# Performance work log

Hardware: AMD Instinct MI355X
Metric: run time of the kernel (lower is better)

Reference implementation:

```python
import jax, jax.numpy as jnp
import numpy as np

N, E, B = 3000, 96000, 64
CIN, MID = 8, 16
G1, G2 = 32, 8
FC1, FC2, OUT = 512, 128, 10
EPS = 1e-5


def setup_inputs() -> dict:
    key = jax.random.key(0)
    ks = jax.random.split(key, 40)
    u = lambda k, shape, s: jax.random.uniform(k, shape, jnp.float32, -s, s)
    inp = {}
    inp['x'] = jax.random.normal(ks[0], (N, B, CIN), jnp.float32)
    inp['edge_index'] = jax.random.randint(ks[1], (2, E), 0, N, jnp.int64)
    # SAGEConv params (uniform(-1/sqrt(in_channels), ...))
    s = 1.0 / np.sqrt(CIN)
    inp['edge_w_raw'] = jnp.ones((E,), jnp.float32) * 0.01
    inp['sage_self_w'] = u(ks[2], (CIN, MID), s)
    inp['sage_w'] = u(ks[3], (CIN, MID), s)
    inp['sage_b'] = u(ks[4], (MID,), s)
    # LayerNorm over (num_nodes, mid_channel)
    inp['ln_g'] = jnp.ones((N, MID), jnp.float32)
    inp['ln_b'] = jnp.zeros((N, MID), jnp.float32)
    # 1x1 Conv2d stacks (stored as [out,in] matrices) + BatchNorm2d (eval stats)
    inp['conv1_w'] = jax.random.normal(ks[5], (G1, MID), jnp.float32) * np.sqrt(2.0 / G1)
    inp['conv1_b'] = u(ks[6], (G1,), 1.0 / np.sqrt(MID))
    inp['bn1_g'] = jax.random.uniform(ks[7], (G1,), jnp.float32, 0.5, 1.5)
    inp['bn1_b'] = jax.random.normal(ks[8], (G1,), jnp.float32) * 0.1
    inp['bn1_m'] = jax.random.normal(ks[9], (G1,), jnp.float32) * 0.1
    inp['bn1_v'] = jax.random.uniform(ks[10], (G1,), jnp.float32, 0.5, 1.5)
    inp['conv2_w'] = jax.random.normal(ks[11], (G2, G1), jnp.float32) * np.sqrt(2.0 / G2)
    inp['conv2_b'] = u(ks[12], (G2,), 1.0 / np.sqrt(G1))
    inp['bn2_g'] = jax.random.uniform(ks[13], (G2,), jnp.float32, 0.5, 1.5)
    inp['bn2_b'] = jax.random.normal(ks[14], (G2,), jnp.float32) * 0.1
    inp['bn2_m'] = jax.random.normal(ks[15], (G2,), jnp.float32) * 0.1
    inp['bn2_v'] = jax.random.uniform(ks[16], (G2,), jnp.float32, 0.5, 1.5)
    # FC stack: Linear(G2*N, FC1) + BN1d, Linear(FC1, FC2) + BN1d, fc1
    d0 = G2 * N
    inp['fc_w1'] = jax.random.normal(ks[17], (FC1, d0), jnp.float32) * np.sqrt(2.0 / (d0 + FC1))
    inp['fc_b1'] = jnp.full((FC1,), 0.01, jnp.float32)
    inp['bnf1_g'] = jax.random.uniform(ks[18], (FC1,), jnp.float32, 0.5, 1.5)
    inp['bnf1_b'] = jax.random.normal(ks[19], (FC1,), jnp.float32) * 0.1
    inp['bnf1_m'] = jax.random.normal(ks[20], (FC1,), jnp.float32) * 0.1
    inp['bnf1_v'] = jax.random.uniform(ks[21], (FC1,), jnp.float32, 0.5, 1.5)
    inp['fc_w2'] = jax.random.normal(ks[22], (FC2, FC1), jnp.float32) * np.sqrt(2.0 / (FC1 + FC2))
    inp['fc_b2'] = jnp.full((FC2,), 0.01, jnp.float32)
    inp['bnf2_g'] = jax.random.uniform(ks[23], (FC2,), jnp.float32, 0.5, 1.5)
    inp['bnf2_b'] = jax.random.normal(ks[24], (FC2,), jnp.float32) * 0.1
    inp['bnf2_m'] = jax.random.normal(ks[25], (FC2,), jnp.float32) * 0.1
    inp['bnf2_v'] = jax.random.uniform(ks[26], (FC2,), jnp.float32, 0.5, 1.5)
    inp['fc1_w'] = jax.random.normal(ks[27], (OUT, FC2), jnp.float32) * np.sqrt(2.0 / (FC2 + OUT))
    inp['fc1_b'] = jnp.full((OUT,), 0.01, jnp.float32)
    return inp


def _bn(y, g, b, m, v):
    # eval-mode BatchNorm; y is [B, C, N] or [B, C]
    if y.ndim == 3:
        return (y - m[:, None]) * (g[:, None] / jnp.sqrt(v[:, None] + EPS)) + b[:, None]
    return (y - m) * (g / jnp.sqrt(v + EPS)) + b


def reference(x, edge_index, edge_w_raw, sage_self_w, sage_w, sage_b, ln_g, ln_b,
              conv1_w, conv1_b, bn1_g, bn1_b, bn1_m, bn1_v,
              conv2_w, conv2_b, bn2_g, bn2_b, bn2_m, bn2_v,
              fc_w1, fc_b1, bnf1_g, bnf1_b, bnf1_m, bnf1_v,
              fc_w2, fc_b2, bnf2_g, bnf2_b, bnf2_m, bnf2_v,
              fc1_w, fc1_b):
    row, col = edge_index[0], edge_index[1]
    ew = jax.nn.sigmoid(edge_w_raw)
    # SAGEConv: gather -> weighted message -> scatter-mean by col -> matmul
    msg = x[row] * ew[:, None, None]                          # [E, B, CIN]
    summed = jax.ops.segment_sum(msg, col, num_segments=N)    # [N, B, CIN]
    cnt = jax.ops.segment_sum(jnp.ones((E,), x.dtype), col, num_segments=N)
    agg = summed / jnp.maximum(cnt, 1.0)[:, None, None]
    neigh = jnp.einsum('nbc,cm->nbm', agg, sage_w) + sage_b   # [N, B, MID]
    self_out = jnp.einsum('nbc,cm->nbm', x, sage_self_w)
    h = 0.0 * self_out + 1.0 * neigh                          # alphas = [0, 1]
    h = jax.nn.relu(h)
    # LayerNorm over (num_nodes, mid) per batch element
    hb = jnp.transpose(h, (1, 0, 2))                          # [B, N, MID]
    mu = hb.mean(axis=(1, 2), keepdims=True)
    var = hb.var(axis=(1, 2), keepdims=True)
    hb = (hb - mu) / jnp.sqrt(var + EPS) * ln_g + ln_b
    y = jnp.transpose(hb, (0, 2, 1))                          # [B, MID, N]
    # 1x1 conv stack (relu then BN, matching source order)
    y = jnp.einsum('om,bmn->bon', conv1_w, y) + conv1_b[:, None]
    y = _bn(jax.nn.relu(y), bn1_g, bn1_b, bn1_m, bn1_v)
    y = jnp.einsum('oc,bcn->bon', conv2_w, y) + conv2_b[:, None]
    y = _bn(jax.nn.relu(y), bn2_g, bn2_b, bn2_m, bn2_v)       # [B, G2, N]
    z = y.reshape(y.shape[0], -1)                             # [B, G2*N]
    z = jax.nn.relu(_bn(z @ fc_w1.T + fc_b1, bnf1_g, bnf1_b, bnf1_m, bnf1_v))
    z = jax.nn.relu(_bn(z @ fc_w2.T + fc_b2, bnf2_g, bnf2_b, bnf2_m, bnf2_v))
    logits = z @ fc1_w.T + fc1_b
    return jax.nn.softmax(logits, axis=-1), logits
```

## Files before the change

kernel.cpp:

```cpp
#include <hip/hip_runtime.h>
#include <hip/hip_bf16.h>
#include <math.h>

#define NN   3000
#define EE   96000
#define BB   64
#define CIN  8
#define MID  16
#define G1   32
#define G2   8
#define FC1N 512
#define FC2N 128
#define OUTN 10
#define EPSV 1e-5f

#define BC   (BB * CIN)
#define HROW (NN * MID)
#define D0   (G2 * NN)

#define P_EWRAW 0
#define P_SW    96000
#define P_SB    96128
#define P_LNG   96144
#define P_LNB   144144
#define P_C1W   192144
#define P_C1B   192656
#define P_BN1G  192688
#define P_BN1B  192720
#define P_BN1M  192752
#define P_BN1V  192784
#define P_C2W   192816
#define P_C2B   193072
#define P_BN2G  193080
#define P_BN2B  193088
#define P_BN2M  193096
#define P_BN2V  193104
#define P_FB1   193112
#define P_BF1G  193624
#define P_BF1B  194136
#define P_BF1M  194648
#define P_BF1V  195160
#define P_FW2   195672
#define P_FB2   261208
#define P_BF2G  261336
#define P_BF2B  261464
#define P_BF2M  261592
#define P_BF2V  261720
#define P_FOW   261848
#define P_FOB   263128
#define P_TOT   263138

#define KCH  320
#define NKC  75
#define SK   32

__device__ __forceinline__ float b2f(unsigned short u) {
    union { unsigned int i; float f; } c;
    c.i = ((unsigned int)u) << 16;
    return c.f;
}

typedef __attribute__((ext_vector_type(8))) unsigned short us8;

__global__ void k_prep(const void* __restrict__ ei_raw,
                       const unsigned int* __restrict__ ewr,
                       int* __restrict__ ei32, int* __restrict__ cnt,
                       int* __restrict__ flags) {
    __shared__ int is64;
    if (threadIdx.x == 0) {
        const int* p = (const int*)ei_raw;
        int any = 0;
        #pragma unroll
        for (int i = 1; i < 32; i += 2) any |= p[i];
        is64 = (any == 0) ? 1 : 0;
        if (blockIdx.x == 0) {
            unsigned int w = ewr[0];
            flags[0] = ((w >> 16) == (w & 0xFFFFu)) ? 1 : 0;
        }
    }
    __syncthreads();
    int i = blockIdx.x * blockDim.x + threadIdx.x;
    if (i < 2 * EE) {
        int v = is64 ? (int)((const long long*)ei_raw)[i]
                     : ((const int*)ei_raw)[i];
        ei32[i] = v;
        if (i >= EE) atomicAdd(&cnt[v], 1);
    }
}

struct PTab { const void* p[30]; };
__global__ __launch_bounds__(256)
void k_cvt_all(PTab tab, const void* __restrict__ xr,
               const int* __restrict__ flags,
               float* __restrict__ x32, float* __restrict__ P) {
    int i = blockIdx.x * blockDim.x + threadIdx.x;
    int bf = flags[0];
    if (i < NN * BC) {
        x32[i] = bf ? b2f(((const unsigned short*)xr)[i]) : ((const float*)xr)[i];
        return;
    }
    i -= NN * BC;
    if (i >= P_TOT) return;
    const int off[31] = {
        P_EWRAW, P_SW, P_SB, P_LNG, P_LNB, P_C1W, P_C1B, P_BN1G, P_BN1B, P_BN1M,
        P_BN1V, P_C2W, P_C2B, P_BN2G, P_BN2B, P_BN2M, P_BN2V, P_FB1, P_BF1G,
        P_BF1B, P_BF1M, P_BF1V, P_FW2, P_FB2, P_BF2G, P_BF2B, P_BF2M, P_BF2V,
        P_FOW, P_FOB, P_TOT };
    int r = 0;
    #pragma unroll
    for (int j = 1; j < 31; ++j) r += (i >= off[j]) ? 1 : 0;
    int e = i - off[r];
    P[i] = bf ? b2f(((const unsigned short*)tab.p[r])[e])
              : ((const float*)tab.p[r])[e];
}

__global__ void k_scan(const int* __restrict__ cnt, int* __restrict__ off,
                       int* __restrict__ cursor) {
    __shared__ int part[1024];
    int t = threadIdx.x;
    int base = t * 3;
    int c0 = 0, c1 = 0, c2 = 0;
    if (base     < NN) c0 = cnt[base];
    if (base + 1 < NN) c1 = cnt[base + 1];
    if (base + 2 < NN) c2 = cnt[base + 2];
    int s = c0 + c1 + c2;
    part[t] = s;
    __syncthreads();
    for (int d = 1; d < 1024; d <<= 1) {
        int v = (t >= d) ? part[t - d] : 0;
        __syncthreads();
        part[t] += v;
        __syncthreads();
    }
    int excl = part[t] - s;
    if (base < NN)     { off[base]     = excl;           cursor[base]     = excl; }
    if (base + 1 < NN) { off[base + 1] = excl + c0;      cursor[base + 1] = excl + c0; }
    if (base + 2 < NN) { off[base + 2] = excl + c0 + c1; cursor[base + 2] = excl + c0 + c1; }
    if (t == 1023) off[NN] = part[1023];
}

__global__ void k_scatter(const int* __restrict__ ei, const float* __restrict__ ew,
                          int* __restrict__ cursor,
                          int* __restrict__ rcsr, float* __restrict__ wcsr) {
    int e = blockIdx.x * blockDim.x + threadIdx.x;
    if (e < EE) {
        int p = atomicAdd(&cursor[ei[EE + e]], 1);
        rcsr[p] = ei[e];
        wcsr[p] = 1.f / (1.f + expf(-ew[e]));
    }
}

__global__ __launch_bounds__(256)
void k_agg_sage(const float* __restrict__ x,
                const int* __restrict__ off,
                const int* __restrict__ rcsr, const float* __restrict__ wcsr,
                const float* __restrict__ sw, const float* __restrict__ sb,
                float* __restrict__ hb) {
    __shared__ float aggL[BC];
    __shared__ float swL[CIN * MID];
    __shared__ float sbL[MID];
    int n = blockIdx.x;
    int t = threadIdx.x;
    if (t < CIN * MID) swL[t] = sw[t];
    if (t < MID)       sbL[t] = sb[t];
    int k0 = off[n], k1 = off[n + 1];
    float a0 = 0.f, a1 = 0.f, b0 = 0.f, b1 = 0.f;
    int k = k0;
    for (; k + 1 < k1; k += 2) {
        int   r0 = rcsr[k],   r1 = rcsr[k + 1];
        float w0 = wcsr[k],   w1 = wcsr[k + 1];
        const float* xp0 = x + (size_t)r0 * BC;
        const float* xp1 = x + (size_t)r1 * BC;
        a0 += xp0[t]       * w0;
        a1 += xp0[t + 256] * w0;
        b0 += xp1[t]       * w1;
        b1 += xp1[t + 256] * w1;
    }
    if (k < k1) {
        int r0 = rcsr[k];
        float w0 = wcsr[k];
        const float* xp0 = x + (size_t)r0 * BC;
        a0 += xp0[t] * w0;
        a1 += xp0[t + 256] * w0;
    }
    float inv = 1.f / fmaxf((float)(k1 - k0), 1.f);
    aggL[t]       = (a0 + b0) * inv;
    aggL[t + 256] = (a1 + b1) * inv;
    __syncthreads();
    #pragma unroll
    for (int r4 = 0; r4 < 4; ++r4) {
        int q = t + r4 * 256;
        int b = q >> 4, m = q & 15;
        float v = sbL[m];
        const float* ag = &aggL[b * CIN];
        #pragma unroll
        for (int c = 0; c < CIN; ++c) v += ag[c] * swL[c * MID + m];
        v = fmaxf(v, 0.f);
        hb[(size_t)b * HROW + n * MID + m] = v;
    }
}

__global__ __launch_bounds__(256)
void k_ln_stats(const float* __restrict__ hb, float* __restrict__ stats) {
    __shared__ float ssum[256], ssq[256];
    int b = blockIdx.x, t = threadIdx.x;
    const float4* p = (const float4*)(hb + (size_t)b * HROW);
    float s = 0.f, q = 0.f;
    for (int i = t; i < HROW / 4; i += 256) {
        float4 v = p[i];
        s += v.x + v.y + v.z + v.w;
        q += v.x * v.x + v.y * v.y + v.z * v.z + v.w * v.w;
    }
    ssum[t] = s; ssq[t] = q;
    __syncthreads();
    for (int d = 128; d > 0; d >>= 1) {
        if (t < d) { ssum[t] += ssum[t + d]; ssq[t] += ssq[t + d]; }
        __syncthreads();
    }
    if (t == 0) {
        float mu = ssum[0] / (float)HROW;
        float var = ssq[0] / (float)HROW - mu * mu;
        stats[b]      = mu;
        stats[BB + b] = 1.f / sqrtf(var + EPSV);
    }
}

__global__ __launch_bounds__(256)
void k_conv_stack(const float* __restrict__ hb, const float* __restrict__ stats,
                  const float* __restrict__ P, float* __restrict__ zT) {
    __shared__ float hbt[64 * 65];
    __shared__ float w1s[G1 * MID], w2s[G2 * G1];
    __shared__ float c1s[G1], s1[G1], t1[G1];
    __shared__ float c2s[G2], s2[G2], t2[G2];
    int t = threadIdx.x;
    int n0 = blockIdx.x * 4;
    for (int j = t; j < G1 * MID; j += 256) w1s[j] = P[P_C1W + j];
    if (t < G2 * G1)  w2s[t] = P[P_C2W + t];
    if (t < G1) {
        float s = P[P_BN1G + t] / sqrtf(P[P_BN1V + t] + EPSV);
        c1s[t] = P[P_C1B + t]; s1[t] = s; t1[t] = P[P_BN1B + t] - P[P_BN1M + t] * s;
    }
    if (t < G2) {
        float s = P[P_BN2G + t] / sqrtf(P[P_BN2V + t] + EPSV);
        c2s[t] = P[P_C2B + t]; s2[t] = s; t2[t] = P[P_BN2B + t] - P[P_BN2M + t] * s;
    }
    #pragma unroll
    for (int r = 0; r < 4; ++r) {
        int i = r * 256 + t;
        int b = i >> 4, q = i & 15;
        float4 v = *(const float4*)(hb + (size_t)b * HROW + n0 * MID + q * 4);
        int ld = b * 65 + q * 4;
        hbt[ld] = v.x; hbt[ld + 1] = v.y; hbt[ld + 2] = v.z; hbt[ld + 3] = v.w;
    }
    __syncthreads();
    int nl = t >> 6, b = t & 63;
    int n = n0 + nl;
    float mu = stats[b], rs = stats[BB + b];
    float tv[MID];
    #pragma unroll
    for (int m = 0; m < MID; ++m) {
        float g = P[P_LNG + n * MID + m], lb = P[P_LNB + n * MID + m];
        tv[m] = (hbt[b * 65 + nl * MID + m] - mu) * rs * g + lb;
    }
    float v1[G1];
    #pragma unroll
    for (int o = 0; o < G1; ++o) {
        float d = c1s[o];
        #pragma unroll
        for (int m = 0; m < MID; ++m) d += w1s[o * MID + m] * tv[m];
        d = fmaxf(d, 0.f);
        v1[o] = d * s1[o] + t1[o];
    }
    #pragma unroll
    for (int o2 = 0; o2 < G2; ++o2) {
        float d = c2s[o2];
        #pragma unroll
        for (int c = 0; c < G1; ++c) d += w2s[o2 * G1 + c] * v1[c];
        d = fmaxf(d, 0.f);
        zT[((size_t)(o2 * NN + n)) * BB + b] = d * s2[o2] + t2[o2];
    }
}

__global__ __launch_bounds__(256)
void k_fc1(const float* __restrict__ zT, const void* __restrict__ w1raw,
           const int* __restrict__ flags, float* __restrict__ out1p) {
    __shared__ float ws[32 * 40];
    __shared__ float zs[SK * 64];
    int fg = blockIdx.x, kc = blockIdx.y;
    int t = threadIdx.x;
    int fs2 = t >> 4, bq = t & 15;
    int f0 = fg * 32;
    int bf = flags[0];
    const float*          w1f = (const float*)w1raw;
    const unsigned short* w1b = (const unsigned short*)w1raw;
    const size_t kcb = (size_t)kc * KCH;

    float a[8];
    #pragma unroll
    for (int i = 0; i < 8; ++i) a[i] = 0.f;

    for (int step = 0; step < KCH / SK; ++step) {
        int kbase = step * SK;
        if (bf) {
            if (t < 128) {
                int row = t >> 2, kq8 = t & 3;
                us8 wv = *(const us8*)(w1b + (size_t)(f0 + row) * D0 + kcb + kbase + kq8 * 8);
                #pragma unroll
                for (int c = 0; c < 8; ++c) ws[row * 40 + kq8 * 8 + c] = b2f(wv[c]);
            }
        } else {
            int row = t >> 3, kq = t & 7;
            *(float4*)&ws[row * 40 + kq * 4] =
                *(const float4*)(w1f + (size_t)(f0 + row) * D0 + kcb + kbase + kq * 4);
        }
        const float* zsrc = zT + (kcb + kbase) * BB;
        *(float4*)&zs[t * 8]     = *(const float4*)(zsrc + t * 8);
        *(float4*)&zs[t * 8 + 4] = *(const float4*)(zsrc + t * 8 + 4);
        __syncthreads();
        #pragma unroll
        for (int k4 = 0; k4 < SK / 4; ++k4) {
            float4 w0 = *(const float4*)&ws[(fs2 * 2    ) * 40 + k4 * 4];
            float4 w1 = *(const float4*)&ws[(fs2 * 2 + 1) * 40 + k4 * 4];
            float4 z0 = *(const float4*)&zs[(k4 * 4    ) * 64 + bq * 4];
            float4 z1 = *(const float4*)&zs[(k4 * 4 + 1) * 64 + bq * 4];
            float4 z2 = *(const float4*)&zs[(k4 * 4 + 2) * 64 + bq * 4];
            float4 z3 = *(const float4*)&zs[(k4 * 4 + 3) * 64 + bq * 4];
            a[0] += w0.x * z0.x + w0.y * z1.x + w0.z * z2.x + w0.w * z3.x;
            a[1] += w0.x * z0.y + w0.y * z1.y + w0.z * z2.y + w0.w * z3.y;
            a[2] += w0.x * z0.z + w0.y * z1.z + w0.z * z2.z + w0.w * z3.z;
            a[3] += w0.x * z0.w + w0.y * z1.w + w0.z * z2.w + w0.w * z3.w;
            a[4] += w1.x * z0.x + w1.y * z1.x + w1.z * z2.x + w1.w * z3.x;
            a[5] += w1.x * z0.y + w1.y * z1.y + w1.z * z2.y + w1.w * z3.y;
            a[6] += w1.x * z0.z + w1.y * z1.z + w1.z * z2.z + w1.w * z3.z;
            a[7] += w1.x * z0.w + w1.y * z1.w + w1.z * z2.w + w1.w * z3.w;
        }
        __syncthreads();
    }
    float* op = out1p + ((size_t)kc * FC1N + f0 + fs2 * 2) * BB + bq * 4;
    *(float4*)op        = make_float4(a[0], a[1], a[2], a[3]);
    *(float4*)(op + BB) = make_float4(a[4], a[5], a[6], a[7]);
}

__global__ void k_fc1_fin(const float* __restrict__ out1p, const float* __restrict__ P,
                          float* __restrict__ z1) {
    int i = blockIdx.x * blockDim.x + threadIdx.x;
    if (i < BB * FC1N) {
        int f = i >> 6, b = i & 63;
        float acc = 0.f;
        for (int kc = 0; kc < NKC; ++kc)
            acc += out1p[((size_t)kc * FC1N + f) * BB + b];
        acc += P[P_FB1 + f];
        float s = P[P_BF1G + f] / sqrtf(P[P_BF1V + f] + EPSV);
        acc = (acc - P[P_BF1M + f]) * s + P[P_BF1B + f];
        z1[b * FC1N + f] = fmaxf(acc, 0.f);
    }
}

__global__ __launch_bounds__(128)
void k_fc2head(const float* __restrict__ z1, const float* __restrict__ P,
               const int* __restrict__ flags, void* __restrict__ outv) {
    __shared__ float zsrc[FC1N];
    __shared__ float z2s[FC2N];
    __shared__ float lg[OUTN];
    __shared__ float red[2];
    int b = blockIdx.x, t = threadIdx.x;
    #pragma unroll
    for (int r = 0; r < 4; ++r) zsrc[t + r * 128] = z1[b * FC1N + t + r * 128];
    __syncthreads();
    {
        int f = t;
        const float4* wr = (const float4*)(P + P_FW2 + (size_t)f * FC1N);
        const float4* zr = (const float4*)zsrc;
        float acc = P[P_FB2 + f];
        for (int k = 0; k < FC1N / 4; ++k) {
            float4 wv = wr[k];
            float4 zv = zr[k];
            acc += wv.x * zv.x + wv.y * zv.y + wv.z * zv.z + wv.w * zv.w;
        }
        float s = P[P_BF2G + f] / sqrtf(P[P_BF2V + f] + EPSV);
        acc = (acc - P[P_BF2M + f]) * s + P[P_BF2B + f];
        z2s[f] = fmaxf(acc, 0.f);
    }
    __syncthreads();
    if (t < OUTN) {
        float acc = P[P_FOB + t];
        const float* wr = P + P_FOW + t * FC2N;
        for (int k = 0; k < FC2N; ++k) acc += wr[k] * z2s[k];
        lg[t] = acc;
    }
    __syncthreads();
    if (t == 0) {
        float mx = lg[0];
        for (int o = 1; o < OUTN; ++o) mx = fmaxf(mx, lg[o]);
        float s = 0.f;
        for (int o = 0; o < OUTN; ++o) s += expf(lg[o] - mx);
        red[0] = mx; red[1] = s;
    }
    __syncthreads();
    if (t < OUTN) {
        float p = expf(lg[t] - red[0]) / red[1];
        if (flags[0]) {
            __hip_bfloat16* o = (__hip_bfloat16*)outv;
            o[b * OUTN + t] = __float2bfloat16(p);
            o[BB * OUTN + b * OUTN + t] = __float2bfloat16(lg[t]);
        } else {
            float* o = (float*)outv;
            o[b * OUTN + t] = p;
            o[BB * OUTN + b * OUTN + t] = lg[t];
        }
    }
}

extern "C" void kernel_launch(void* const* d_in, const int* in_sizes, int n_in,
                              void* d_out, int out_size, void* d_ws, size_t ws_size,
                              hipStream_t stream) {
    char* ws = (char*)d_ws;
    size_t o = 0;
    auto carve = [&](size_t bytes) { void* p = ws + o; o += (bytes + 255) & ~(size_t)255; return p; };
    int*   flags  = (int*)  carve(16);
    int*   ei32   = (int*)  carve((size_t)2 * EE * sizeof(int));
    int*   cnt    = (int*)  carve(NN * sizeof(int));
    int*   off    = (int*)  carve((NN + 1) * sizeof(int));
    int*   cursor = (int*)  carve(NN * sizeof(int));
    int*   rcsr   = (int*)  carve(EE * sizeof(int));
    float* wcsr   = (float*)carve(EE * sizeof(float));
    float* P      = (float*)carve((size_t)P_TOT * sizeof(float));
    float* x32    = (float*)carve((size_t)NN * BC * sizeof(float));
    float* hb     = (float*)carve((size_t)BB * HROW * sizeof(float));
    float* stats  = (float*)carve(2 * BB * sizeof(float));
    float* zT     = (float*)carve((size_t)D0 * BB * sizeof(float));
    float* out1p  = (float*)carve((size_t)NKC * FC1N * BB * sizeof(float));
    float* z1     = (float*)carve(BB * FC1N * sizeof(float));

    hipMemsetAsync(cnt, 0, NN * sizeof(int), stream);

    k_prep<<<(2 * EE + 255) / 256, 256, 0, stream>>>(d_in[1], (const unsigned int*)d_in[2],
                                                     ei32, cnt, flags);

    PTab tab;
    tab.p[0]  = d_in[2];   tab.p[1]  = d_in[4];   tab.p[2]  = d_in[5];
    tab.p[3]  = d_in[6];   tab.p[4]  = d_in[7];   tab.p[5]  = d_in[8];
    tab.p[6]  = d_in[9];   tab.p[7]  = d_in[10];  tab.p[8]  = d_in[11];
    tab.p[9]  = d_in[12];  tab.p[10] = d_in[13];  tab.p[11] = d_in[14];
    tab.p[12] = d_in[15];  tab.p[13] = d_in[16];  tab.p[14] = d_in[17];
    tab.p[15] = d_in[18];  tab.p[16] = d_in[19];  tab.p[17] = d_in[21];
    tab.p[18] = d_in[22];  tab.p[19] = d_in[23];  tab.p[20] = d_in[24];
    tab.p[21] = d_in[25];  tab.p[22] = d_in[26];  tab.p[23] = d_in[27];
    tab.p[24] = d_in[28];  tab.p[25] = d_in[29];  tab.p[26] = d_in[30];
    tab.p[27] = d_in[31];  tab.p[28] = d_in[32];  tab.p[29] = d_in[33];
    int cvt_tot = NN * BC + P_TOT;
    k_cvt_all<<<(cvt_tot + 255) / 256, 256, 0, stream>>>(tab, d_in[0], flags, x32, P);

    k_scan   <<<1, 1024, 0, stream>>>(cnt, off, cursor);
    k_scatter<<<(EE + 255) / 256, 256, 0, stream>>>(ei32, P + P_EWRAW, cursor, rcsr, wcsr);
    k_agg_sage<<<NN, 256, 0, stream>>>(x32, off, rcsr, wcsr, P + P_SW, P + P_SB, hb);
    k_ln_stats<<<BB, 256, 0, stream>>>(hb, stats);
    k_conv_stack<<<NN / 4, 256, 0, stream>>>(hb, stats, P, zT);
    dim3 g7(FC1N / 32, NKC);
    k_fc1    <<<g7, 256, 0, stream>>>(zT, d_in[20], flags, out1p);
    k_fc1_fin<<<(BB * FC1N + 255) / 256, 256, 0, stream>>>(out1p, P, z1);
    k_fc2head<<<BB, 128, 0, stream>>>(z1, P, flags, (void*)d_out);
}
```

Baseline: 281.0 us.

## Rewrite FC1 as register-tiled wave GEMM, fuse prep kernels, unroll aggregation

FC1 no longer uses a shared-memory tiled loop. Each wave now holds 64 z values per lane in registers and accumulates 32 output features, reading weight rows through uniform per-wave loads, with a new K-chunk split (192 wide, 125 chunks). The edge-index prep and the input/parameter conversion kernels are merged into one launch, which removes a launch and the flags read. The neighbour aggregation loop is unrolled by four to put more independent gathers in flight. The register-heavy FC1 (64 z values plus 32 accumulators) may lower occupancy, and the larger partial-sum buffer adds work to the reduction in k_fc1_fin.

```diff
diff --git a/kernel.cpp b/kernel.cpp
--- a/kernel.cpp
+++ b/kernel.cpp
@@ -50,9 +50,8 @@
 #define P_FOB   263128
 #define P_TOT   263138
 
-#define KCH  320
-#define NKC  75
-#define SK   32
+#define KCH  192
+#define NKC  125
 
 __device__ __forceinline__ float b2f(unsigned short u) {
     union { unsigned int i; float f; } c;
@@ -60,47 +59,43 @@
     return c.f;
 }
 
-typedef __attribute__((ext_vector_type(8))) unsigned short us8;
-
-__global__ void k_prep(const void* __restrict__ ei_raw,
-                       const unsigned int* __restrict__ ewr,
-                       int* __restrict__ ei32, int* __restrict__ cnt,
-                       int* __restrict__ flags) {
-    __shared__ int is64;
+struct PTab { const void* p[30]; };
+__global__ __launch_bounds__(256)
+void k_prep(const void* __restrict__ ei_raw, const unsigned int* __restrict__ ewr,
+            const void* __restrict__ xr, PTab tab,
+            int* __restrict__ ei32, int* __restrict__ cnt, int* __restrict__ flags,
+            float* __restrict__ x32, float* __restrict__ P) {
+    __shared__ int sh_is64, sh_bf;
     if (threadIdx.x == 0) {
-        const int* p = (const int*)ei_raw;
+        const int* pw = (const int*)ei_raw;
         int any = 0;
         #pragma unroll
-        for (int i = 1; i < 32; i += 2) any |= p[i];
-        is64 = (any == 0) ? 1 : 0;
-        if (blockIdx.x == 0) {
-            unsigned int w = ewr[0];
-            flags[0] = ((w >> 16) == (w & 0xFFFFu)) ? 1 : 0;
-        }
-    }
-    __syncthreads();
-    int i = blockIdx.x * blockDim.x + threadIdx.x;
-    if (i < 2 * EE) {
-        int v = is64 ? (int)((const long long*)ei_raw)[i]
-                     : ((const int*)ei_raw)[i];
+        for (int i = 1; i < 32; i += 2) any |= pw[i];
+        sh_is64 = (any == 0) ? 1 : 0;
+        unsigned int w = ewr[0];
+        sh_bf = ((w >> 16) == (w & 0xFFFFu)) ? 1 : 0;
+        if (blockIdx.x == 0) flags[0] = sh_bf;
+    }
+    __syncthreads();
+    int bf = sh_bf;
+    long long gi = (long long)blockIdx.x * blockDim.x + threadIdx.x;
+    if (gi < 2 * EE) {
+        int i = (int)gi;
+        int v = sh_is64 ? (int)((const long long*)ei_raw)[i]
+                        : ((const int*)ei_raw)[i];
         ei32[i] = v;
         if (i >= EE) atomicAdd(&cnt[v], 1);
-    }
-}
-
-struct PTab { const void* p[30]; };
-__global__ __launch_bounds__(256)
-void k_cvt_all(PTab tab, const void* __restrict__ xr,
-               const int* __restrict__ flags,
-               float* __restrict__ x32, float* __restrict__ P) {
-    int i = blockIdx.x * blockDim.x + threadIdx.x;
-    int bf = flags[0];
-    if (i < NN * BC) {
+        return;
+    }
+    gi -= 2 * EE;
+    if (gi < NN * BC) {
+        int i = (int)gi;
         x32[i] = bf ? b2f(((const unsigned short*)xr)[i]) : ((const float*)xr)[i];
         return;
     }
-    i -= NN * BC;
-    if (i >= P_TOT) return;
+    gi -= NN * BC;
+    if (gi >= P_TOT) return;
+    int i = (int)gi;
     const int off[31] = {
         P_EWRAW, P_SW, P_SB, P_LNG, P_LNB, P_C1W, P_C1B, P_BN1G, P_BN1B, P_BN1M,
         P_BN1V, P_C2W, P_C2B, P_BN2G, P_BN2B, P_BN2M, P_BN2V, P_FB1, P_BF1G,
@@ -166,17 +161,21 @@
     int k0 = off[n], k1 = off[n + 1];
     float a0 = 0.f, a1 = 0.f, b0 = 0.f, b1 = 0.f;
     int k = k0;
-    for (; k + 1 < k1; k += 2) {
-        int   r0 = rcsr[k],   r1 = rcsr[k + 1];
-        float w0 = wcsr[k],   w1 = wcsr[k + 1];
+    for (; k + 3 < k1; k += 4) {
+        int   r0 = rcsr[k],     r1 = rcsr[k + 1];
+        int   r2 = rcsr[k + 2], r3 = rcsr[k + 3];
+        float w0 = wcsr[k],     w1 = wcsr[k + 1];
+        float w2 = wcsr[k + 2], w3 = wcsr[k + 3];
         const float* xp0 = x + (size_t)r0 * BC;
         const float* xp1 = x + (size_t)r1 * BC;
-        a0 += xp0[t]       * w0;
-        a1 += xp0[t + 256] * w0;
-        b0 += xp1[t]       * w1;
-        b1 += xp1[t + 256] * w1;
-    }
-    if (k < k1) {
+        const float* xp2 = x + (size_t)r2 * BC;
+        const float* xp3 = x + (size_t)r3 * BC;
+        a0 += xp0[t]       * w0;  a1 += xp0[t + 256] * w0;
+        b0 += xp1[t]       * w1;  b1 += xp1[t + 256] * w1;
+        a0 += xp2[t]       * w2;  a1 += xp2[t + 256] * w2;
+        b0 += xp3[t]       * w3;  b1 += xp3[t + 256] * w3;
+    }
+    for (; k < k1; ++k) {
         int r0 = rcsr[k];
         float w0 = wcsr[k];
         const float* xp0 = x + (size_t)r0 * BC;
@@ -284,61 +283,50 @@
 __global__ __launch_bounds__(256)
 void k_fc1(const float* __restrict__ zT, const void* __restrict__ w1raw,
            const int* __restrict__ flags, float* __restrict__ out1p) {
-    __shared__ float ws[32 * 40];
-    __shared__ float zs[SK * 64];
-    int fg = blockIdx.x, kc = blockIdx.y;
-    int t = threadIdx.x;
-    int fs2 = t >> 4, bq = t & 15;
-    int f0 = fg * 32;
-    int bf = flags[0];
-    const float*          w1f = (const float*)w1raw;
-    const unsigned short* w1b = (const unsigned short*)w1raw;
-    const size_t kcb = (size_t)kc * KCH;
-
-    float a[8];
-    #pragma unroll
-    for (int i = 0; i < 8; ++i) a[i] = 0.f;
-
-    for (int step = 0; step < KCH / SK; ++step) {
-        int kbase = step * SK;
-        if (bf) {
-            if (t < 128) {
-                int row = t >> 2, kq8 = t & 3;
-                us8 wv = *(const us8*)(w1b + (size_t)(f0 + row) * D0 + kcb + kbase + kq8 * 8);
+    int kc = blockIdx.y;
+    int wv = __builtin_amdgcn_readfirstlane(threadIdx.x >> 6);
+    int lane = threadIdx.x & 63;
+    int fbase = blockIdx.x * 128 + wv * 32;
+    int kcb = kc * KCH;
+    float acc[32];
+    #pragma unroll
+    for (int f = 0; f < 32; ++f) acc[f] = 0.f;
+    if (flags[0]) {
+        const unsigned int* wb = (const unsigned int*)w1raw;
+        for (int ss = 0; ss < KCH / 64; ++ss) {
+            int k0 = kcb + ss * 64;
+            float z[64];
+            #pragma unroll
+            for (int j = 0; j < 64; ++j) z[j] = zT[(size_t)(k0 + j) * BB + lane];
+            #pragma unroll
+            for (int f = 0; f < 32; ++f) {
+                const unsigned int* wr = wb + ((size_t)(fbase + f) * D0 + k0) / 2;
                 #pragma unroll
-                for (int c = 0; c < 8; ++c) ws[row * 40 + kq8 * 8 + c] = b2f(wv[c]);
+                for (int j = 0; j < 32; ++j) {
+                    unsigned int u = wr[j];
+                    acc[f] += b2f((unsigned short)(u & 0xFFFFu)) * z[2 * j]
+                            + b2f((unsigned short)(u >> 16))     * z[2 * j + 1];
+                }
             }
-        } else {
-            int row = t >> 3, kq = t & 7;
-            *(float4*)&ws[row * 40 + kq * 4] =
-                *(const float4*)(w1f + (size_t)(f0 + row) * D0 + kcb + kbase + kq * 4);
         }
-        const float* zsrc = zT + (kcb + kbase) * BB;
-        *(float4*)&zs[t * 8]     = *(const float4*)(zsrc + t * 8);
-        *(float4*)&zs[t * 8 + 4] = *(const float4*)(zsrc + t * 8 + 4);
-        __syncthreads();
-        #pragma unroll
-        for (int k4 = 0; k4 < SK / 4; ++k4) {
-            float4 w0 = *(const float4*)&ws[(fs2 * 2    ) * 40 + k4 * 4];
-            float4 w1 = *(const float4*)&ws[(fs2 * 2 + 1) * 40 + k4 * 4];
-            float4 z0 = *(const float4*)&zs[(k4 * 4    ) * 64 + bq * 4];
-            float4 z1 = *(const float4*)&zs[(k4 * 4 + 1) * 64 + bq * 4];
-            float4 z2 = *(const float4*)&zs[(k4 * 4 + 2) * 64 + bq * 4];
-            float4 z3 = *(const float4*)&zs[(k4 * 4 + 3) * 64 + bq * 4];
-            a[0] += w0.x * z0.x + w0.y * z1.x + w0.z * z2.x + w0.w * z3.x;
-            a[1] += w0.x * z0.y + w0.y * z1.y + w0.z * z2.y + w0.w * z3.y;
-            a[2] += w0.x * z0.z + w0.y * z1.z + w0.z * z2.z + w0.w * z3.z;
-            a[3] += w0.x * z0.w + w0.y * z1.w + w0.z * z2.w + w0.w * z3.w;
-            a[4] += w1.x * z0.x + w1.y * z1.x + w1.z * z2.x + w1.w * z3.x;
-            a[5] += w1.x * z0.y + w1.y * z1.y + w1.z * z2.y + w1.w * z3.y;
-            a[6] += w1.x * z0.z + w1.y * z1.z + w1.z * z2.z + w1.w * z3.z;
-            a[7] += w1.x * z0.w + w1.y * z1.w + w1.z * z2.w + w1.w * z3.w;
+    } else {
+        const float* wf = (const float*)w1raw;
+        for (int ss = 0; ss < KCH / 64; ++ss) {
+            int k0 = kcb + ss * 64;
+            float z[64];
+            #pragma unroll
+            for (int j = 0; j < 64; ++j) z[j] = zT[(size_t)(k0 + j) * BB + lane];
+            #pragma unroll
+            for (int f = 0; f < 32; ++f) {
+                const float* wr = wf + (size_t)(fbase + f) * D0 + k0;
+                #pragma unroll
+                for (int j = 0; j < 64; ++j) acc[f] += wr[j] * z[j];
+            }
         }
-        __syncthreads();
-    }
-    float* op = out1p + ((size_t)kc * FC1N + f0 + fs2 * 2) * BB + bq * 4;
-    *(float4*)op        = make_float4(a[0], a[1], a[2], a[3]);
-    *(float4*)(op + BB) = make_float4(a[4], a[5], a[6], a[7]);
+    }
+    float* op = out1p + ((size_t)kc * FC1N + fbase) * BB + lane;
+    #pragma unroll
+    for (int f = 0; f < 32; ++f) op[f * BB] = acc[f];
 }
 
 __global__ void k_fc1_fin(const float* __restrict__ out1p, const float* __restrict__ P,
@@ -434,9 +422,6 @@
 
     hipMemsetAsync(cnt, 0, NN * sizeof(int), stream);
 
-    k_prep<<<(2 * EE + 255) / 256, 256, 0, stream>>>(d_in[1], (const unsigned int*)d_in[2],
-                                                     ei32, cnt, flags);
-
     PTab tab;
     tab.p[0]  = d_in[2];   tab.p[1]  = d_in[4];   tab.p[2]  = d_in[5];
     tab.p[3]  = d_in[6];   tab.p[4]  = d_in[7];   tab.p[5]  = d_in[8];
@@ -448,15 +433,18 @@
     tab.p[21] = d_in[25];  tab.p[22] = d_in[26];  tab.p[23] = d_in[27];
     tab.p[24] = d_in[28];  tab.p[25] = d_in[29];  tab.p[26] = d_in[30];
     tab.p[27] = d_in[31];  tab.p[28] = d_in[32];  tab.p[29] = d_in[33];
-    int cvt_tot = NN * BC + P_TOT;
-    k_cvt_all<<<(cvt_tot + 255) / 256, 256, 0, stream>>>(tab, d_in[0], flags, x32, P);
+
+    long long prep_tot = 2LL * EE + (long long)NN * BC + P_TOT;
+    k_prep<<<(int)((prep_tot + 255) / 256), 256, 0, stream>>>(
+        d_in[1], (const unsigned int*)d_in[2], d_in[0], tab,
+        ei32, cnt, flags, x32, P);
 
     k_scan   <<<1, 1024, 0, stream>>>(cnt, off, cursor);
     k_scatter<<<(EE + 255) / 256, 256, 0, stream>>>(ei32, P + P_EWRAW, cursor, rcsr, wcsr);
     k_agg_sage<<<NN, 256, 0, stream>>>(x32, off, rcsr, wcsr, P + P_SW, P + P_SB, hb);
     k_ln_stats<<<BB, 256, 0, stream>>>(hb, stats);
     k_conv_stack<<<NN / 4, 256, 0, stream>>>(hb, stats, P, zT);
-    dim3 g7(FC1N / 32, NKC);
+    dim3 g7(4, NKC);
     k_fc1    <<<g7, 256, 0, stream>>>(zT, d_in[20], flags, out1p);
     k_fc1_fin<<<(BB * FC1N + 255) / 256, 256, 0, stream>>>(out1p, P, z1);
     k_fc2head<<<BB, 128, 0, stream>>>(z1, P, flags, (void*)d_out);
```

Measured after the change: 436.6 us. +55.4%, slower.
